# Kernel tuning notes

Measured on AMD Instinct MI355X. Metric: run time of the kernel, lower is better.

## Reference

```python
import jax, jax.numpy as jnp
import numpy as np

B, T, D = 1, 256, 512
H, DH = 8, 64
INIT = 0.02
IGNORE = -1e6


def setup_inputs() -> dict:
    key = jax.random.key(0)
    ks = jax.random.split(key, 6)
    return {
        "x": jax.random.normal(ks[0], (B, T, D), jnp.float32),
        "W_kkqvv": jax.random.normal(ks[1], (D, 5 * H * DH), jnp.float32) * INIT,
        "b_kkqvv": jnp.zeros((5 * H * DH,), jnp.float32),
        "W_Kq": jax.random.normal(ks[2], (H, DH, DH, DH), jnp.float32) * INIT,
        "W_Vq": jax.random.normal(ks[3], (H, DH, DH, DH), jnp.float32) * INIT,
        "W_out": jax.random.normal(ks[4], (H * DH, D), jnp.float32) * INIT,
        "b_out": jnp.zeros((D,), jnp.float32),
    }


def reference(x, W_kkqvv, b_kkqvv, W_Kq, W_Vq, W_out, b_out):
    b, t, d = x.shape
    proj = x @ W_kkqvv + b_kkqvv                     # [b, t, 5*H*DH]
    k1, k2, q, v1, v2 = jnp.split(proj, 5, axis=-1)
    resh = lambda a: a.reshape(b, t, H, DH).transpose(0, 2, 1, 3)  # [b, h, t, dh]
    k1, k2, q, v1, v2 = map(resh, (k1, k2, q, v1, v2))

    # bilinear value tensor: v[b,n,p,s,e] = sum_{a,c} v1[b,n,p,a] v2[b,n,s,c] W_Vq[n,a,c,e]
    v = jnp.einsum('bnpa,bnsc,nace->bnpse', v1, v2, W_Vq)
    v = v.transpose(0, 1, 4, 2, 3).reshape(b, H, DH, t * t)       # [b, n, dh, p*s]

    # trilinear score: step1[b,n,p,t,i] then contract with q over i
    step1 = jnp.einsum('bnpk,bntj,nkji->bnpti', k1, k2, W_Kq)
    attn = jnp.einsum('bnpti,bnqi->bnptq', step1, q)              # [b, n, p, t, q]

    # causal mask: p > q or t > q  ->  IGNORE
    idx = jnp.arange(t)
    mask = (idx[:, None, None] > idx[None, None, :]) | (idx[None, :, None] > idx[None, None, :])
    attn = jnp.where(mask[None, None], IGNORE, attn)

    attn = attn.transpose(0, 1, 4, 2, 3).reshape(b, H, t, t * t) / DH  # [b, n, q, p*t]
    attn = jax.nn.softmax(attn, axis=-1)

    z = jnp.einsum('bnql,bnhl->bqnh', attn, v)                     # [b, q, n, dh]
    return z.reshape(b, t, H * DH) @ W_out + b_out
```

## Files before the change

### kernel.cpp

```cpp
#include <hip/hip_runtime.h>

typedef unsigned short u16;
typedef unsigned int u32;
typedef __attribute__((ext_vector_type(8))) short bf16x8;
typedef __attribute__((ext_vector_type(4))) float f32x4;
#define MFMA __builtin_amdgcn_mfma_f32_16x16x32_bf16

#define TT 256
#define DD 512
#define HH 8
#define DHH 64
#define NC 2560

__device__ __forceinline__ u16 f2bf(float f) {
    u32 x; __builtin_memcpy(&x, &f, 4);
    u32 r = (x + 0x7FFFu + ((x >> 16) & 1u)) >> 16;
    return (u16)r;
}
__device__ __forceinline__ void unpack2(u32 u, float& lo, float& hi) {
    u32 l = u << 16, h = u & 0xFFFF0000u;
    __builtin_memcpy(&lo, &l, 4); __builtin_memcpy(&hi, &h, 4);
}

__global__ __launch_bounds__(256) void prep2_kernel(
    const float* __restrict__ W1, const float* __restrict__ Wo,
    const float* __restrict__ x,
    const float* __restrict__ WK, const float* __restrict__ WV,
    u16* __restrict__ Wt, u16* __restrict__ Wot, u16* __restrict__ xb,
    u16* __restrict__ WKt, u16* __restrict__ WVt) {
    __shared__ float S[64 * 65];
    const int bid = blockIdx.x, tid = threadIdx.x;
    if (bid < 384) {
        int tc, tr, Cw;
        const float* src; u16* dst;
        if (bid < 320) { tc = bid % 40; tr = bid / 40; src = W1; dst = Wt;  Cw = 2560; }
        else { int b2 = bid - 320; tc = b2 % 8; tr = b2 / 8; src = Wo; dst = Wot; Cw = 512; }
        {
            int X = tid >> 2, c0 = (tid & 3) * 16;
            const float4* s4 = (const float4*)(src + (size_t)(tr * 64 + X) * Cw + tc * 64 + c0);
            float4 v0 = s4[0], v1 = s4[1], v2 = s4[2], v3 = s4[3];
            float* d = &S[X * 65 + c0];
            d[0]=v0.x; d[1]=v0.y; d[2]=v0.z; d[3]=v0.w;
            d[4]=v1.x; d[5]=v1.y; d[6]=v1.z; d[7]=v1.w;
            d[8]=v2.x; d[9]=v2.y; d[10]=v2.z; d[11]=v2.w;
            d[12]=v3.x; d[13]=v3.y; d[14]=v3.z; d[15]=v3.w;
        }
        __syncthreads();
        {
            int Y = tid >> 2, x0 = (tid & 3) * 16;
            __attribute__((aligned(16))) u16 tmp[16];
#pragma unroll
            for (int xx = 0; xx < 16; ++xx) tmp[xx] = f2bf(S[(x0 + xx) * 65 + Y]);
            u16* o = dst + (size_t)(tc * 64 + Y) * 512 + tr * 64 + x0;
            *(uint4*)o = *(uint4*)tmp;
            *(uint4*)(o + 8) = *(uint4*)(tmp + 8);
        }
    } else if (bid < 392) {
        int b3 = bid - 384;
        size_t base = (size_t)(b3 * 256 + tid) * 64;
        const float4* s = (const float4*)(x + base);
#pragma unroll
        for (int i = 0; i < 8; ++i) {
            float4 lo = s[2 * i], hi = s[2 * i + 1];
            __attribute__((aligned(16))) u16 t8[8];
            t8[0]=f2bf(lo.x); t8[1]=f2bf(lo.y); t8[2]=f2bf(lo.z); t8[3]=f2bf(lo.w);
            t8[4]=f2bf(hi.x); t8[5]=f2bf(hi.y); t8[6]=f2bf(hi.z); t8[7]=f2bf(hi.w);
            ((uint4*)(xb + base))[i] = *(uint4*)t8;
        }
    } else {
        const int b2 = bid - 392;
        const int outer = b2 & 63, n = (b2 >> 6) & 7, which = b2 >> 9;
        const float* in = (which ? WV : WK) + ((size_t)(n * 64 + outer)) * 4096;
        u16* outbase = (which ? WVt : WKt) + (size_t)n * 262144;
        {
            int X = tid >> 2, c0 = (tid & 3) * 16;
            const float4* s = (const float4*)(in + X * 64 + c0);
            float4 v0 = s[0], v1 = s[1], v2 = s[2], v3 = s[3];
            float* d = &S[X * 65 + c0];
            d[0]=v0.x; d[1]=v0.y; d[2]=v0.z; d[3]=v0.w;
            d[4]=v1.x; d[5]=v1.y; d[6]=v1.z; d[7]=v1.w;
            d[8]=v2.x; d[9]=v2.y; d[10]=v2.z; d[11]=v2.w;
            d[12]=v3.x; d[13]=v3.y; d[14]=v3.z; d[15]=v3.w;
        }
        __syncthreads();
        {
            int Y = tid >> 2, x0 = (tid & 3) * 16;
            __attribute__((aligned(16))) u16 tmp[16];
#pragma unroll
            for (int xx = 0; xx < 16; ++xx) tmp[xx] = f2bf(S[(x0 + xx) * 65 + Y]);
            u16* d = outbase + (size_t)Y * 4096 + (size_t)outer * 64 + x0;
            *(uint4*)d = *(uint4*)tmp;
            *(uint4*)(d + 8) = *(uint4*)(tmp + 8);
        }
    }
}

__global__ __launch_bounds__(256) void proj_mfma(
    const u16* __restrict__ xb, const u16* __restrict__ Wt,
    const float* __restrict__ bias, u16* __restrict__ fiveb, u16* __restrict__ v1T) {
    __shared__ float R[3][16][68];
    const int tid = threadIdx.x, w = tid >> 6, lane = tid & 63;
    const int quad = lane >> 4, l15 = lane & 15;
    const int m0 = blockIdx.x * 16;
    const int c0 = blockIdx.y * 64;
    const int k0 = w * 128;
    f32x4 acc[4];
#pragma unroll
    for (int nt = 0; nt < 4; ++nt) acc[nt] = (f32x4){0.f, 0.f, 0.f, 0.f};
#pragma unroll
    for (int kc = 0; kc < 4; ++kc) {
        bf16x8 a = *(const bf16x8*)&xb[(size_t)(m0 + l15) * 512 + k0 + kc * 32 + quad * 8];
#pragma unroll
        for (int nt = 0; nt < 4; ++nt) {
            bf16x8 b = *(const bf16x8*)&Wt[(size_t)(c0 + nt * 16 + l15) * 512 + k0 + kc * 32 + quad * 8];
            acc[nt] = MFMA(a, b, acc[nt], 0, 0, 0);
        }
    }
    if (w > 0) {
#pragma unroll
        for (int nt = 0; nt < 4; ++nt)
#pragma unroll
            for (int r = 0; r < 4; ++r)
                R[w - 1][quad * 4 + r][nt * 16 + l15] = acc[nt][r];
    }
    __syncthreads();
    if (w == 0) {
#pragma unroll
        for (int nt = 0; nt < 4; ++nt) {
            const int col = c0 + nt * 16 + l15;
            const float b = bias[col];
            const int v = col >> 9, h = (col >> 6) & 7, e = col & 63;
#pragma unroll
            for (int r = 0; r < 4; ++r) {
                const int row = quad * 4 + r;
                float s = acc[nt][r] + R[0][row][nt * 16 + l15]
                        + R[1][row][nt * 16 + l15] + R[2][row][nt * 16 + l15];
                const int t = m0 + row;
                u16 val = f2bf(s + b);
                if (v == 3) v1T[(h * 64 + e) * 256 + t] = val;
                else        fiveb[((v * 8 + h) * 256 + t) * 64 + e] = val;
            }
        }
    }
}

__global__ __launch_bounds__(256) void mu_gemm(
    const u16* __restrict__ fiveb, const u16* __restrict__ WKt,
    const u16* __restrict__ WVt, u16* __restrict__ M_all, u16* __restrict__ U_all) {
    __shared__ u16 Cst[64 * 64];
    const int f0 = blockIdx.x * 64, n = blockIdx.y, which = blockIdx.z;
    const u16* vec = fiveb + ((which ? 4 : 1) * HH + n) * TT * DHH;
    const u16* W = (which ? WVt : WKt) + (size_t)n * 262144;
    u16* out = (which ? U_all : M_all) + (size_t)n * 262144;
    const int tid = threadIdx.x, w = tid >> 6, lane = tid & 63;
    const int quad = lane >> 4, l15 = lane & 15;

    const bf16x8 a0 = *(const bf16x8*)&vec[(w * 16 + l15) * 64 + quad * 8];
    const bf16x8 a1 = *(const bf16x8*)&vec[(w * 16 + l15) * 64 + 32 + quad * 8];
#pragma unroll
    for (int nt = 0; nt < 4; ++nt) {
        bf16x8 b0 = *(const bf16x8*)&W[(size_t)(f0 + nt * 16 + l15) * 64 + quad * 8];
        bf16x8 b1 = *(const bf16x8*)&W[(size_t)(f0 + nt * 16 + l15) * 64 + 32 + quad * 8];
        f32x4 c = {0.f, 0.f, 0.f, 0.f};
        c = MFMA(a0, b0, c, 0, 0, 0);
        c = MFMA(a1, b1, c, 0, 0, 0);
#pragma unroll
        for (int r = 0; r < 4; ++r)
            Cst[(w * 16 + quad * 4 + r) * 64 + nt * 16 + l15] = f2bf(c[r]);
    }
    __syncthreads();
    const int row = tid >> 2, cc = (tid & 3) * 16;
    const uint4* src = (const uint4*)&Cst[row * 64 + cc];
    uint4* dst = (uint4*)(out + (size_t)row * 4096 + f0 + cc);
    dst[0] = src[0]; dst[1] = src[1];
}

__global__ __launch_bounds__(256) void km_gemm(
    const u16* __restrict__ fiveb, const u16* __restrict__ M_all, u16* __restrict__ KM) {
    __shared__ u16 Cst[256 * 64];
    const int t = blockIdx.x, n = blockIdx.y;
    const u16* k1 = fiveb + (0 * HH + n) * TT * DHH;
    const u16* Mt = M_all + (size_t)n * 262144 + (size_t)t * 4096;
    const int tid = threadIdx.x, w = tid >> 6, lane = tid & 63;
    const int quad = lane >> 4, l15 = lane & 15;

    bf16x8 bf[4][2];
#pragma unroll
    for (int nt = 0; nt < 4; ++nt) {
        bf[nt][0] = *(const bf16x8*)&Mt[(nt * 16 + l15) * 64 + quad * 8];
        bf[nt][1] = *(const bf16x8*)&Mt[(nt * 16 + l15) * 64 + 32 + quad * 8];
    }
#pragma unroll
    for (int mt = 0; mt < 4; ++mt) {
        const int prow = w * 64 + mt * 16 + l15;
        bf16x8 a0 = *(const bf16x8*)&k1[prow * 64 + quad * 8];
        bf16x8 a1 = *(const bf16x8*)&k1[prow * 64 + 32 + quad * 8];
#pragma unroll
        for (int nt = 0; nt < 4; ++nt) {
            f32x4 c = {0.f, 0.f, 0.f, 0.f};
            c = MFMA(a0, bf[nt][0], c, 0, 0, 0);
            c = MFMA(a1, bf[nt][1], c, 0, 0, 0);
#pragma unroll
            for (int r = 0; r < 4; ++r)
                Cst[(w * 64 + mt * 16 + quad * 4 + r) * 64 + nt * 16 + l15] = f2bf(c[r]);
        }
    }
    __syncthreads();
    const uint4* src = (const uint4*)&Cst[tid * 64];
    uint4* dst = (uint4*)(KM + ((size_t)(n * 64 + t) * 256 + (size_t)tid) * 64);
#pragma unroll
    for (int i = 0; i < 8; ++i) dst[i] = src[i];
}

__global__ __launch_bounds__(256, 4) void main_kernel(
    const u16* __restrict__ fiveb, const u16* __restrict__ v1T,
    const u16* __restrict__ KM, const u16* __restrict__ U_all,
    u16* __restrict__ Zpart, float* __restrict__ Lpart) {
    __shared__ u16 Sb_all[4 * 1152];
    const int tid = threadIdx.x;
    const int b = blockIdx.x;
    const int qt = 3 - (b >> 9);
    const int r = b & 511, n = r >> 6, t = r & 63;
    const int w = tid >> 6, lane = tid & 63, quad = lane >> 4, l15 = lane & 15;
    const int nP = qt + 1;
    const int qrow0 = qt * 64 + w * 16;

    const u16* qg  = fiveb + (2 * HH + n) * 16384;
    const u16* v1g = v1T + n * 16384;
    const u16* KMt = KM + (size_t)n * 1048576 + (size_t)t * 16384;
    const u16* Ut  = U_all + (size_t)n * 262144 + (size_t)t * 4096;
    u16* Sb = Sb_all + w * 1152;

    const bf16x8 qa0 = *(const bf16x8*)&qg[(qrow0 + l15) * 64 + quad * 8];
    const bf16x8 qa1 = *(const bf16x8*)&qg[(qrow0 + l15) * 64 + 32 + quad * 8];

    bf16x8 ones;
    { uint4 ou = {0x3F803F80u, 0x3F803F80u, 0x3F803F80u, 0x3F803F80u};
      __builtin_memcpy(&ones, &ou, 16); }

    f32x4 G[4];
#pragma unroll
    for (int nt = 0; nt < 4; ++nt) G[nt] = (f32x4){0.f, 0.f, 0.f, 0.f};
    f32x4 Lacc = {0.f, 0.f, 0.f, 0.f};

    for (int pt = 0; pt < nP; ++pt) {
#pragma unroll
        for (int nt = 0; nt < 4; ++nt) {
            const int p = pt * 64 + nt * 16 + l15;
            bf16x8 b0 = *(const bf16x8*)&KMt[(size_t)p * 64 + quad * 8];
            bf16x8 b1 = *(const bf16x8*)&KMt[(size_t)p * 64 + 32 + quad * 8];
            f32x4 s = {0.f, 0.f, 0.f, 0.f};
            s = MFMA(qa0, b0, s, 0, 0, 0);
            s = MFMA(qa1, b1, s, 0, 0, 0);
#pragma unroll
            for (int rr = 0; rr < 4; ++rr) {
                const int q = qrow0 + quad * 4 + rr;
                float wv = (p <= q && t <= q) ? __expf(s[rr] * 0.015625f) : 0.f;
                Sb[(quad * 4 + rr) * 72 + nt * 16 + l15] = f2bf(wv);
            }
        }
        bf16x8 pa0 = *(const bf16x8*)&Sb[l15 * 72 + quad * 8];
        bf16x8 pa1 = *(const bf16x8*)&Sb[l15 * 72 + 32 + quad * 8];
        Lacc = MFMA(pa0, ones, Lacc, 0, 0, 0);
        Lacc = MFMA(pa1, ones, Lacc, 0, 0, 0);
#pragma unroll
        for (int nt = 0; nt < 4; ++nt) {
            bf16x8 b0 = *(const bf16x8*)&v1g[(nt * 16 + l15) * 256 + pt * 64 + quad * 8];
            bf16x8 b1 = *(const bf16x8*)&v1g[(nt * 16 + l15) * 256 + pt * 64 + 32 + quad * 8];
            G[nt] = MFMA(pa0, b0, G[nt], 0, 0, 0);
            G[nt] = MFMA(pa1, b1, G[nt], 0, 0, 0);
        }
    }
#pragma unroll
    for (int nt = 0; nt < 4; ++nt)
#pragma unroll
        for (int rr = 0; rr < 4; ++rr)
            Sb[(quad * 4 + rr) * 72 + nt * 16 + l15] = f2bf(G[nt][rr]);
    bf16x8 ga0 = *(const bf16x8*)&Sb[l15 * 72 + quad * 8];
    bf16x8 ga1 = *(const bf16x8*)&Sb[l15 * 72 + 32 + quad * 8];
    f32x4 Zacc[4];
#pragma unroll
    for (int nt = 0; nt < 4; ++nt) {
        bf16x8 b0 = *(const bf16x8*)&Ut[(nt * 16 + l15) * 64 + quad * 8];
        bf16x8 b1 = *(const bf16x8*)&Ut[(nt * 16 + l15) * 64 + 32 + quad * 8];
        f32x4 c = {0.f, 0.f, 0.f, 0.f};
        c = MFMA(ga0, b0, c, 0, 0, 0);
        Zacc[nt] = MFMA(ga1, b1, c, 0, 0, 0);
    }

#pragma unroll
    for (int nt = 0; nt < 4; ++nt)
#pragma unroll
        for (int rr = 0; rr < 4; ++rr)
            Sb[(quad * 4 + rr) * 72 + nt * 16 + l15] = f2bf(Zacc[nt][rr]);
    {
        const int row = lane >> 2, cc = (lane & 3) * 16;
        uint4 z0 = *(const uint4*)&Sb[row * 72 + cc];
        uint4 z1 = *(const uint4*)&Sb[row * 72 + cc + 8];
        uint4* d = (uint4*)(Zpart + (size_t)b * 4096 + (w * 16 + row) * 64 + cc);
        d[0] = z0; d[1] = z1;
    }
    if (l15 == 0) {
        float4 lv;
        lv.x = Lacc[0]; lv.y = Lacc[1]; lv.z = Lacc[2]; lv.w = Lacc[3];
        *(float4*)(Lpart + b * 64 + w * 16 + quad * 4) = lv;
    }
}

__global__ __launch_bounds__(256) void zn_kernel(
    const u16* __restrict__ Zpart, const float* __restrict__ Lpart, u16* __restrict__ zn) {
    __shared__ float LS[16][17];
    const int bid = blockIdx.x;
    const int group = bid >> 2, quarter = bid & 3;
    const int qtd = group >> 3, h = group & 7;
    const int qt = 3 - qtd;
    const int s0 = qtd * 512 + h * 64;
    const int tid = threadIdx.x;
    const int qq = quarter * 16 + (tid >> 4);
    const int e  = (tid & 15) * 4;

    const u16* src = Zpart + (size_t)s0 * 4096 + qq * 64 + e;
    float a0 = 0.f, a1 = 0.f, a2 = 0.f, a3 = 0.f;
    for (int t = 0; t < 64; ++t) {
        uint2 zv = *(const uint2*)(src + (size_t)t * 4096);
        float f0, f1, f2, f3;
        unpack2(zv.x, f0, f1); unpack2(zv.y, f2, f3);
        a0 += f0; a1 += f1; a2 += f2; a3 += f3;
    }
    {
        const int qq_l = tid >> 4, tc = tid & 15;
        const float* lp = Lpart + (size_t)(s0 + tc * 4) * 64 + quarter * 16 + qq_l;
        LS[qq_l][tc] = lp[0] + lp[64] + lp[128] + lp[192];
    }
    __syncthreads();
    float Ls = 0.f;
    {
        const int qq_l = tid >> 4;
#pragma unroll
        for (int j2 = 0; j2 < 16; ++j2) Ls += LS[qq_l][j2];
    }
    const float inv = 1.f / Ls;
    __attribute__((aligned(8))) u16 t4[4];
    t4[0] = f2bf(a0 * inv); t4[1] = f2bf(a1 * inv);
    t4[2] = f2bf(a2 * inv); t4[3] = f2bf(a3 * inv);
    *(uint2*)(zn + (size_t)(qt * 64 + qq) * 512 + h * 64 + e) = *(uint2*)t4;
}

__global__ __launch_bounds__(256) void out_mfma(
    const u16* __restrict__ zn, const u16* __restrict__ Wot,
    const float* __restrict__ b_out, float* __restrict__ out) {
    __shared__ float R[3][16][68];
    const int tid = threadIdx.x, w = tid >> 6, lane = tid & 63;
    const int quad = lane >> 4, l15 = lane & 15;
    const int m0 = blockIdx.x * 16;
    const int c0 = blockIdx.y * 64;
    const int k0 = w * 128;
    f32x4 acc[4];
#pragma unroll
    for (int nt = 0; nt < 4; ++nt) acc[nt] = (f32x4){0.f, 0.f, 0.f, 0.f};
#pragma unroll
    for (int kc = 0; kc < 4; ++kc) {
        bf16x8 a = *(const bf16x8*)&zn[(size_t)(m0 + l15) * 512 + k0 + kc * 32 + quad * 8];
#pragma unroll
        for (int nt = 0; nt < 4; ++nt) {
            bf16x8 b = *(const bf16x8*)&Wot[(size_t)(c0 + nt * 16 + l15) * 512 + k0 + kc * 32 + quad * 8];
            acc[nt] = MFMA(a, b, acc[nt], 0, 0, 0);
        }
    }
    if (w > 0) {
#pragma unroll
        for (int nt = 0; nt < 4; ++nt)
#pragma unroll
            for (int r = 0; r < 4; ++r)
                R[w - 1][quad * 4 + r][nt * 16 + l15] = acc[nt][r];
    }
    __syncthreads();
    if (w == 0) {
#pragma unroll
        for (int nt = 0; nt < 4; ++nt) {
            const int col = c0 + nt * 16 + l15;
            const float b = b_out[col];
#pragma unroll
            for (int r = 0; r < 4; ++r) {
                const int row = quad * 4 + r;
                float s = acc[nt][r] + R[0][row][nt * 16 + l15]
                        + R[1][row][nt * 16 + l15] + R[2][row][nt * 16 + l15];
                out[(size_t)(m0 + row) * 512 + col] = s + b;
            }
        }
    }
}

extern "C" void kernel_launch(void* const* d_in, const int* in_sizes, int n_in,
                              void* d_out, int out_size, void* d_ws, size_t ws_size,
                              hipStream_t stream) {
    const float* x       = (const float*)d_in[0];
    const float* W_kkqvv = (const float*)d_in[1];
    const float* b_kkqvv = (const float*)d_in[2];
    const float* W_Kq    = (const float*)d_in[3];
    const float* W_Vq    = (const float*)d_in[4];
    const float* W_out   = (const float*)d_in[5];
    const float* b_out   = (const float*)d_in[6];

    char* base = (char*)d_ws;
    u16*   fiveb = (u16*)(base + 0);
    u16*   U_all = (u16*)(base + 1310720);
    u16*   KM    = (u16*)(base + 5505024);
    u16*   Zpart = (u16*)(base + 22282240);
    u16*   Wot   = (u16*)(base + 39059456);
    u16*   v1T   = (u16*)(base + 39583744);
    u16*   zn    = (u16*)(base + 39845888);
    float* Lpart = (float*)(base + 40108032);
    u16*   M_all = (u16*)(base + 22282240);
    u16*   WKt   = (u16*)(base + 26476544);
    u16*   WVt   = (u16*)(base + 30670848);
    u16*   Wt    = (u16*)(base + 34865152);
    u16*   xb    = (u16*)(base + 37486592);

    prep2_kernel<<<1416, 256, 0, stream>>>(W_kkqvv, W_out, x, W_Kq, W_Vq,
                                           Wt, Wot, xb, WKt, WVt);
    proj_mfma<<<dim3(16, 40), 256, 0, stream>>>(xb, Wt, b_kkqvv, fiveb, v1T);
    mu_gemm<<<dim3(64, 8, 2), 256, 0, stream>>>(fiveb, WKt, WVt, M_all, U_all);
    km_gemm<<<dim3(64, 8), 256, 0, stream>>>(fiveb, M_all, KM);
    main_kernel<<<2048, 256, 0, stream>>>(fiveb, v1T, KM, U_all, Zpart, Lpart);
    zn_kernel<<<128, 256, 0, stream>>>(Zpart, Lpart, zn);
    out_mfma<<<dim3(16, 8), 256, 0, stream>>>(zn, Wot, b_out, (float*)d_out);
}
```

Baseline: 172.1 us.

## Fuse KM GEMM into main attention kernel, keeping KM tiles in LDS

Removes the separate km_gemm kernel, which wrote a 16 MB KM tensor to global memory for main_kernel to read back. Each 512-thread block now handles one (head, t) pair, computes the k1·M product into swizzled shared memory, then loops over all four q tiles from there. Shared-memory layouts use an XOR swizzle to avoid bank conflicts. In exchange, parallelism drops from 2048 to 512 blocks, blocks take unequal causal work, and more __syncthreads are needed per tile.

```diff
diff --git a/kernel.cpp b/kernel.cpp
--- a/kernel.cpp
+++ b/kernel.cpp
@@ -20,6 +20,9 @@
 __device__ __forceinline__ void unpack2(u32 u, float& lo, float& hi) {
     u32 l = u << 16, h = u & 0xFFFF0000u;
     __builtin_memcpy(&lo, &l, 4); __builtin_memcpy(&hi, &h, 4);
+}
+__device__ __forceinline__ int swz(int row, int col) {
+    return (row * 64 + col) ^ ((row & 7) << 3);
 }
 
 __global__ __launch_bounds__(256) void prep2_kernel(
@@ -175,135 +178,132 @@
     dst[0] = src[0]; dst[1] = src[1];
 }
 
-__global__ __launch_bounds__(256) void km_gemm(
-    const u16* __restrict__ fiveb, const u16* __restrict__ M_all, u16* __restrict__ KM) {
-    __shared__ u16 Cst[256 * 64];
-    const int t = blockIdx.x, n = blockIdx.y;
-    const u16* k1 = fiveb + (0 * HH + n) * TT * DHH;
-    const u16* Mt = M_all + (size_t)n * 262144 + (size_t)t * 4096;
-    const int tid = threadIdx.x, w = tid >> 6, lane = tid & 63;
-    const int quad = lane >> 4, l15 = lane & 15;
-
-    bf16x8 bf[4][2];
-#pragma unroll
-    for (int nt = 0; nt < 4; ++nt) {
-        bf[nt][0] = *(const bf16x8*)&Mt[(nt * 16 + l15) * 64 + quad * 8];
-        bf[nt][1] = *(const bf16x8*)&Mt[(nt * 16 + l15) * 64 + 32 + quad * 8];
-    }
-#pragma unroll
-    for (int mt = 0; mt < 4; ++mt) {
-        const int prow = w * 64 + mt * 16 + l15;
-        bf16x8 a0 = *(const bf16x8*)&k1[prow * 64 + quad * 8];
-        bf16x8 a1 = *(const bf16x8*)&k1[prow * 64 + 32 + quad * 8];
-#pragma unroll
-        for (int nt = 0; nt < 4; ++nt) {
-            f32x4 c = {0.f, 0.f, 0.f, 0.f};
-            c = MFMA(a0, bf[nt][0], c, 0, 0, 0);
-            c = MFMA(a1, bf[nt][1], c, 0, 0, 0);
-#pragma unroll
-            for (int r = 0; r < 4; ++r)
-                Cst[(w * 64 + mt * 16 + quad * 4 + r) * 64 + nt * 16 + l15] = f2bf(c[r]);
-        }
-    }
-    __syncthreads();
-    const uint4* src = (const uint4*)&Cst[tid * 64];
-    uint4* dst = (uint4*)(KM + ((size_t)(n * 64 + t) * 256 + (size_t)tid) * 64);
-#pragma unroll
-    for (int i = 0; i < 8; ++i) dst[i] = src[i];
-}
-
-__global__ __launch_bounds__(256, 4) void main_kernel(
+__global__ __launch_bounds__(512, 2) void main_fused(
     const u16* __restrict__ fiveb, const u16* __restrict__ v1T,
-    const u16* __restrict__ KM, const u16* __restrict__ U_all,
+    const u16* __restrict__ M_all, const u16* __restrict__ U_all,
     u16* __restrict__ Zpart, float* __restrict__ Lpart) {
-    __shared__ u16 Sb_all[4 * 1152];
+    __shared__ __attribute__((aligned(16))) u16 KMb[4][4096];
+    __shared__ __attribute__((aligned(16))) u16 PLb[4][1024];
+    __shared__ __attribute__((aligned(16))) u16 GLb[4][1024];
     const int tid = threadIdx.x;
-    const int b = blockIdx.x;
-    const int qt = 3 - (b >> 9);
-    const int r = b & 511, n = r >> 6, t = r & 63;
+    const int b = blockIdx.x, n = b & 7, t = b >> 3;
     const int w = tid >> 6, lane = tid & 63, quad = lane >> 4, l15 = lane & 15;
-    const int nP = qt + 1;
-    const int qrow0 = qt * 64 + w * 16;
-
-    const u16* qg  = fiveb + (2 * HH + n) * 16384;
+    const int s = w & 3, h2 = w >> 2;
+
+    const u16* k1g = fiveb + (0 * HH + n) * TT * DHH;
+    const u16* qg  = fiveb + (2 * HH + n) * TT * DHH;
     const u16* v1g = v1T + n * 16384;
-    const u16* KMt = KM + (size_t)n * 1048576 + (size_t)t * 16384;
+    const u16* Mt  = M_all + (size_t)n * 262144 + (size_t)t * 4096;
     const u16* Ut  = U_all + (size_t)n * 262144 + (size_t)t * 4096;
-    u16* Sb = Sb_all + w * 1152;
-
-    const bf16x8 qa0 = *(const bf16x8*)&qg[(qrow0 + l15) * 64 + quad * 8];
-    const bf16x8 qa1 = *(const bf16x8*)&qg[(qrow0 + l15) * 64 + 32 + quad * 8];
 
     bf16x8 ones;
     { uint4 ou = {0x3F803F80u, 0x3F803F80u, 0x3F803F80u, 0x3F803F80u};
       __builtin_memcpy(&ones, &ou, 16); }
 
-    f32x4 G[4];
-#pragma unroll
-    for (int nt = 0; nt < 4; ++nt) G[nt] = (f32x4){0.f, 0.f, 0.f, 0.f};
-    f32x4 Lacc = {0.f, 0.f, 0.f, 0.f};
-
-    for (int pt = 0; pt < nP; ++pt) {
-#pragma unroll
-        for (int nt = 0; nt < 4; ++nt) {
-            const int p = pt * 64 + nt * 16 + l15;
-            bf16x8 b0 = *(const bf16x8*)&KMt[(size_t)p * 64 + quad * 8];
-            bf16x8 b1 = *(const bf16x8*)&KMt[(size_t)p * 64 + 32 + quad * 8];
-            f32x4 s = {0.f, 0.f, 0.f, 0.f};
-            s = MFMA(qa0, b0, s, 0, 0, 0);
-            s = MFMA(qa1, b1, s, 0, 0, 0);
-#pragma unroll
-            for (int rr = 0; rr < 4; ++rr) {
-                const int q = qrow0 + quad * 4 + rr;
-                float wv = (p <= q && t <= q) ? __expf(s[rr] * 0.015625f) : 0.f;
-                Sb[(quad * 4 + rr) * 72 + nt * 16 + l15] = f2bf(wv);
+    const bf16x8 mb00 = *(const bf16x8*)&Mt[(h2 * 32 + l15) * 64 + quad * 8];
+    const bf16x8 mb01 = *(const bf16x8*)&Mt[(h2 * 32 + l15) * 64 + 32 + quad * 8];
+    const bf16x8 mb10 = *(const bf16x8*)&Mt[(h2 * 32 + 16 + l15) * 64 + quad * 8];
+    const bf16x8 mb11 = *(const bf16x8*)&Mt[(h2 * 32 + 16 + l15) * 64 + 32 + quad * 8];
+
+    for (int qt = 0; qt < 4; ++qt) {
+        {
+            const int prow = qt * 64 + s * 16 + l15;
+            bf16x8 a0 = *(const bf16x8*)&k1g[prow * 64 + quad * 8];
+            bf16x8 a1 = *(const bf16x8*)&k1g[prow * 64 + 32 + quad * 8];
+            f32x4 c0 = {0.f, 0.f, 0.f, 0.f}, c1 = {0.f, 0.f, 0.f, 0.f};
+            c0 = MFMA(a0, mb00, c0, 0, 0, 0);
+            c0 = MFMA(a1, mb01, c0, 0, 0, 0);
+            c1 = MFMA(a0, mb10, c1, 0, 0, 0);
+            c1 = MFMA(a1, mb11, c1, 0, 0, 0);
+#pragma unroll
+            for (int r = 0; r < 4; ++r) {
+                const int pl = s * 16 + quad * 4 + r;
+                KMb[qt][swz(pl, h2 * 32 + l15)]      = f2bf(c0[r]);
+                KMb[qt][swz(pl, h2 * 32 + 16 + l15)] = f2bf(c1[r]);
             }
         }
-        bf16x8 pa0 = *(const bf16x8*)&Sb[l15 * 72 + quad * 8];
-        bf16x8 pa1 = *(const bf16x8*)&Sb[l15 * 72 + 32 + quad * 8];
-        Lacc = MFMA(pa0, ones, Lacc, 0, 0, 0);
-        Lacc = MFMA(pa1, ones, Lacc, 0, 0, 0);
-#pragma unroll
-        for (int nt = 0; nt < 4; ++nt) {
-            bf16x8 b0 = *(const bf16x8*)&v1g[(nt * 16 + l15) * 256 + pt * 64 + quad * 8];
-            bf16x8 b1 = *(const bf16x8*)&v1g[(nt * 16 + l15) * 256 + pt * 64 + 32 + quad * 8];
-            G[nt] = MFMA(pa0, b0, G[nt], 0, 0, 0);
-            G[nt] = MFMA(pa1, b1, G[nt], 0, 0, 0);
-        }
-    }
-#pragma unroll
-    for (int nt = 0; nt < 4; ++nt)
-#pragma unroll
-        for (int rr = 0; rr < 4; ++rr)
-            Sb[(quad * 4 + rr) * 72 + nt * 16 + l15] = f2bf(G[nt][rr]);
-    bf16x8 ga0 = *(const bf16x8*)&Sb[l15 * 72 + quad * 8];
-    bf16x8 ga1 = *(const bf16x8*)&Sb[l15 * 72 + 32 + quad * 8];
-    f32x4 Zacc[4];
-#pragma unroll
-    for (int nt = 0; nt < 4; ++nt) {
-        bf16x8 b0 = *(const bf16x8*)&Ut[(nt * 16 + l15) * 64 + quad * 8];
-        bf16x8 b1 = *(const bf16x8*)&Ut[(nt * 16 + l15) * 64 + 32 + quad * 8];
-        f32x4 c = {0.f, 0.f, 0.f, 0.f};
-        c = MFMA(ga0, b0, c, 0, 0, 0);
-        Zacc[nt] = MFMA(ga1, b1, c, 0, 0, 0);
-    }
-
-#pragma unroll
-    for (int nt = 0; nt < 4; ++nt)
-#pragma unroll
-        for (int rr = 0; rr < 4; ++rr)
-            Sb[(quad * 4 + rr) * 72 + nt * 16 + l15] = f2bf(Zacc[nt][rr]);
-    {
-        const int row = lane >> 2, cc = (lane & 3) * 16;
-        uint4 z0 = *(const uint4*)&Sb[row * 72 + cc];
-        uint4 z1 = *(const uint4*)&Sb[row * 72 + cc + 8];
-        uint4* d = (uint4*)(Zpart + (size_t)b * 4096 + (w * 16 + row) * 64 + cc);
-        d[0] = z0; d[1] = z1;
-    }
-    if (l15 == 0) {
-        float4 lv;
-        lv.x = Lacc[0]; lv.y = Lacc[1]; lv.z = Lacc[2]; lv.w = Lacc[3];
-        *(float4*)(Lpart + b * 64 + w * 16 + quad * 4) = lv;
+        const int qrow = qt * 64 + s * 16 + l15;
+        const bf16x8 qa0 = *(const bf16x8*)&qg[qrow * 64 + quad * 8];
+        const bf16x8 qa1 = *(const bf16x8*)&qg[qrow * 64 + 32 + quad * 8];
+        __syncthreads();
+
+        f32x4 G0 = {0.f, 0.f, 0.f, 0.f}, G1 = {0.f, 0.f, 0.f, 0.f};
+        f32x4 Lacc = {0.f, 0.f, 0.f, 0.f};
+        const int qv = qt * 64 + s * 16 + quad * 4;
+
+        for (int pt = 0; pt <= qt; ++pt) {
+#pragma unroll
+            for (int ntc = 0; ntc < 2; ++ntc) {
+                const int pl = (h2 * 2 + ntc) * 16 + l15;
+                bf16x8 b0 = *(const bf16x8*)&KMb[pt][swz(pl, quad * 8)];
+                bf16x8 b1 = *(const bf16x8*)&KMb[pt][swz(pl, 32 + quad * 8)];
+                f32x4 s4 = {0.f, 0.f, 0.f, 0.f};
+                s4 = MFMA(qa0, b0, s4, 0, 0, 0);
+                s4 = MFMA(qa1, b1, s4, 0, 0, 0);
+                const int p = pt * 64 + pl;
+#pragma unroll
+                for (int rr = 0; rr < 4; ++rr) {
+                    const int q = qv + rr;
+                    float wv = (p <= q && t <= q) ? __expf(s4[rr] * 0.015625f) : 0.f;
+                    PLb[s][swz(quad * 4 + rr, pl)] = f2bf(wv);
+                }
+            }
+            const bf16x8 vb00 = *(const bf16x8*)&v1g[((h2 * 2) * 16 + l15) * 256 + pt * 64 + quad * 8];
+            const bf16x8 vb01 = *(const bf16x8*)&v1g[((h2 * 2) * 16 + l15) * 256 + pt * 64 + 32 + quad * 8];
+            const bf16x8 vb10 = *(const bf16x8*)&v1g[((h2 * 2 + 1) * 16 + l15) * 256 + pt * 64 + quad * 8];
+            const bf16x8 vb11 = *(const bf16x8*)&v1g[((h2 * 2 + 1) * 16 + l15) * 256 + pt * 64 + 32 + quad * 8];
+            __syncthreads();
+            const bf16x8 pa0 = *(const bf16x8*)&PLb[s][swz(l15, quad * 8)];
+            const bf16x8 pa1 = *(const bf16x8*)&PLb[s][swz(l15, 32 + quad * 8)];
+            if (h2 == 0) {
+                Lacc = MFMA(pa0, ones, Lacc, 0, 0, 0);
+                Lacc = MFMA(pa1, ones, Lacc, 0, 0, 0);
+            }
+            G0 = MFMA(pa0, vb00, G0, 0, 0, 0);
+            G0 = MFMA(pa1, vb01, G0, 0, 0, 0);
+            G1 = MFMA(pa0, vb10, G1, 0, 0, 0);
+            G1 = MFMA(pa1, vb11, G1, 0, 0, 0);
+            if (pt < qt) __syncthreads();
+        }
+
+#pragma unroll
+        for (int rr = 0; rr < 4; ++rr) {
+            const int ql = quad * 4 + rr;
+            GLb[s][swz(ql, h2 * 32 + l15)]      = f2bf(G0[rr]);
+            GLb[s][swz(ql, h2 * 32 + 16 + l15)] = f2bf(G1[rr]);
+        }
+        const bf16x8 ub00 = *(const bf16x8*)&Ut[((h2 * 2) * 16 + l15) * 64 + quad * 8];
+        const bf16x8 ub01 = *(const bf16x8*)&Ut[((h2 * 2) * 16 + l15) * 64 + 32 + quad * 8];
+        const bf16x8 ub10 = *(const bf16x8*)&Ut[((h2 * 2 + 1) * 16 + l15) * 64 + quad * 8];
+        const bf16x8 ub11 = *(const bf16x8*)&Ut[((h2 * 2 + 1) * 16 + l15) * 64 + 32 + quad * 8];
+        __syncthreads();
+        const bf16x8 ga0 = *(const bf16x8*)&GLb[s][swz(l15, quad * 8)];
+        const bf16x8 ga1 = *(const bf16x8*)&GLb[s][swz(l15, 32 + quad * 8)];
+        f32x4 Z0 = {0.f, 0.f, 0.f, 0.f}, Z1 = {0.f, 0.f, 0.f, 0.f};
+        Z0 = MFMA(ga0, ub00, Z0, 0, 0, 0);
+        Z0 = MFMA(ga1, ub01, Z0, 0, 0, 0);
+        Z1 = MFMA(ga0, ub10, Z1, 0, 0, 0);
+        Z1 = MFMA(ga1, ub11, Z1, 0, 0, 0);
+
+        u16* zp = &PLb[0][0];
+#pragma unroll
+        for (int rr = 0; rr < 4; ++rr) {
+            const int ql = quad * 4 + rr;
+            zp[s * 1024 + ql * 64 + h2 * 32 + l15]      = f2bf(Z0[rr]);
+            zp[s * 1024 + ql * 64 + h2 * 32 + 16 + l15] = f2bf(Z1[rr]);
+        }
+        const int slot = (3 - qt) * 512 + n * 64 + t;
+        __syncthreads();
+        {
+            const uint4* srcv = (const uint4*)zp;
+            uint4* dstv = (uint4*)(Zpart + (size_t)slot * 4096);
+            dstv[tid] = srcv[tid];
+        }
+        if (h2 == 0 && l15 == 0) {
+            float4 lv;
+            lv.x = Lacc[0]; lv.y = Lacc[1]; lv.z = Lacc[2]; lv.w = Lacc[3];
+            *(float4*)(Lpart + (size_t)slot * 64 + s * 16 + quad * 4) = lv;
+        }
     }
 }
 
@@ -405,24 +405,22 @@
     char* base = (char*)d_ws;
     u16*   fiveb = (u16*)(base + 0);
     u16*   U_all = (u16*)(base + 1310720);
-    u16*   KM    = (u16*)(base + 5505024);
-    u16*   Zpart = (u16*)(base + 22282240);
-    u16*   Wot   = (u16*)(base + 39059456);
-    u16*   v1T   = (u16*)(base + 39583744);
-    u16*   zn    = (u16*)(base + 39845888);
-    float* Lpart = (float*)(base + 40108032);
-    u16*   M_all = (u16*)(base + 22282240);
-    u16*   WKt   = (u16*)(base + 26476544);
-    u16*   WVt   = (u16*)(base + 30670848);
-    u16*   Wt    = (u16*)(base + 34865152);
-    u16*   xb    = (u16*)(base + 37486592);
+    u16*   M_all = (u16*)(base + 5505024);
+    u16*   Zpart = (u16*)(base + 9699328);
+    u16*   Wot   = (u16*)(base + 26476544);
+    u16*   v1T   = (u16*)(base + 27000832);
+    u16*   zn    = (u16*)(base + 27262976);
+    float* Lpart = (float*)(base + 27525120);
+    u16*   WKt   = (u16*)(base + 9699328);
+    u16*   WVt   = (u16*)(base + 13893632);
+    u16*   Wt    = (u16*)(base + 18087936);
+    u16*   xb    = (u16*)(base + 20709376);
 
     prep2_kernel<<<1416, 256, 0, stream>>>(W_kkqvv, W_out, x, W_Kq, W_Vq,
                                            Wt, Wot, xb, WKt, WVt);
     proj_mfma<<<dim3(16, 40), 256, 0, stream>>>(xb, Wt, b_kkqvv, fiveb, v1T);
     mu_gemm<<<dim3(64, 8, 2), 256, 0, stream>>>(fiveb, WKt, WVt, M_all, U_all);
-    km_gemm<<<dim3(64, 8), 256, 0, stream>>>(fiveb, M_all, KM);
-    main_kernel<<<2048, 256, 0, stream>>>(fiveb, v1T, KM, U_all, Zpart, Lpart);
+    main_fused<<<512, 512, 0, stream>>>(fiveb, v1T, M_all, U_all, Zpart, Lpart);
     zn_kernel<<<128, 256, 0, stream>>>(Zpart, Lpart, zn);
     out_mfma<<<dim3(16, 8), 256, 0, stream>>>(zn, Wot, b_out, (float*)d_out);
 }
```

Result: faster. 154.0 us (-10.5%).
